# Performance work log

Measured on AMD Instinct MI355X. Metric: run time of the kernel, lower is better.

## Reference

```python
import jax, jax.numpy as jnp
import numpy as np

HEADS = 16
EMBED = 1024
HEAD_DIM = EMBED // HEADS


def setup_inputs() -> dict:
    key = jax.random.key(0)
    ks = jax.random.split(key, 10)
    B, SQ, SKV = 2, 2048, 2048
    s = 1.0 / np.sqrt(HEAD_DIM)
    sd = 1.0 / np.sqrt(EMBED)
    return {
        "queries": jax.random.normal(ks[0], (B, SQ, EMBED), jnp.float32),
        "values": jax.random.normal(ks[1], (B, SKV, EMBED), jnp.float32),
        "heads": HEADS,
        "Wv": jax.random.normal(ks[2], (HEAD_DIM, HEAD_DIM), jnp.float32) * s,
        "bv": jax.random.normal(ks[3], (HEAD_DIM,), jnp.float32) * 0.02,
        "Wk": jax.random.normal(ks[4], (HEAD_DIM, HEAD_DIM), jnp.float32) * s,
        "bk": jax.random.normal(ks[5], (HEAD_DIM,), jnp.float32) * 0.02,
        "Wq": jax.random.normal(ks[6], (HEAD_DIM, HEAD_DIM), jnp.float32) * s,
        "bq": jax.random.normal(ks[7], (HEAD_DIM,), jnp.float32) * 0.02,
        "Wd": jax.random.normal(ks[8], (EMBED, EMBED), jnp.float32) * sd,
        "bd": jax.random.normal(ks[9], (EMBED,), jnp.float32) * 0.02,
    }


def reference(queries, values, heads, Wv, bv, Wk, bk, Wq, bq, Wd, bd):
    n, sq, e = queries.shape
    skv = values.shape[1]
    d = e // heads
    # reshape to per-head layout [b, s, h, d]
    q_in = queries.reshape(n, sq, heads, d)
    v_in = values.reshape(n, skv, heads, d)
    # shared per-head linear projections (torch Linear: x @ W.T + b)
    v = jnp.einsum("bshd,ed->bshe", v_in, Wv) + bv
    # quirk preserved: keys computed from the ALREADY-PROJECTED values
    k = jnp.einsum("bshd,ed->bshe", v, Wk) + bk
    q = jnp.einsum("bshd,ed->bshe", q_in, Wq) + bq
    # full O(n^2) score matrix [b, h, sq, skv] (as in source)
    scores = jnp.einsum("bqhd,bkhd->bhqk", q, k) / jnp.sqrt(jnp.asarray(d, q.dtype))
    attn = jax.nn.softmax(scores, axis=-1)
    out = jnp.einsum("bhqk,bkhd->bqhd", attn, v).reshape(n, sq, e)
    return out @ Wd.T + bd
```

## Files before the change

kernel.cpp:

```cpp
#include <hip/hip_runtime.h>
#include <hip/hip_bf16.h>
#include <hip/hip_fp16.h>
#include <math.h>

typedef _Float16 f16;
typedef _Float16 f16x8 __attribute__((ext_vector_type(8)));
typedef _Float16 f16x4 __attribute__((ext_vector_type(4)));
typedef _Float16 f16x2 __attribute__((ext_vector_type(2)));
typedef unsigned short u16x8v __attribute__((ext_vector_type(8)));
typedef float f32x4 __attribute__((ext_vector_type(4)));

namespace {
constexpr int B = 2;
constexpr int H = 16;
constexpr int S = 2048;
constexpr int D = 64;
constexpr int E = 1024;
constexpr float QSCALE = 0.125f * 1.4426950408889634f;
}

#define GLOBAL_LOAD_LDS16(gp, lp)                                              \
  __builtin_amdgcn_global_load_lds(                                            \
      (const __attribute__((address_space(1))) void*)(gp),                     \
      (__attribute__((address_space(3))) void*)(lp), 16, 0, 0)

__global__ __launch_bounds__(256) void prep(const float* __restrict__ Wd, f16* __restrict__ wd16,
                                            const float* __restrict__ Wk, const float* __restrict__ Wv,
                                            const float* __restrict__ bv, const float* __restrict__ bk,
                                            float* __restrict__ Wkv, float* __restrict__ bkv) {
  if (blockIdx.x < 1024) {
    const int i = blockIdx.x * 256 + threadIdx.x;
    const float4 f = ((const float4*)Wd)[i];
    f16x4 o;
    o.x = (f16)f.x; o.y = (f16)f.y; o.z = (f16)f.z; o.w = (f16)f.w;
    *(f16x4*)(wd16 + 4 * (size_t)i) = o;
  } else {
    const int g = (blockIdx.x - 1024) * 256 + threadIdx.x;
    const int i = g >> 6, j = g & 63;
    float s = 0.f;
#pragma unroll 16
    for (int d = 0; d < 64; ++d) s = fmaf(Wk[i * 64 + d], Wv[d * 64 + j], s);
    Wkv[g] = s;
    if (g < 64) {
      float bb = bk[g];
#pragma unroll 16
      for (int d = 0; d < 64; ++d) bb = fmaf(Wk[g * 64 + d], bv[d], bb);
      bkv[g] = bb;
    }
  }
}

__global__ __launch_bounds__(256) void proj3_mfma(const float* __restrict__ xq,
                                                  const float* __restrict__ xv,
                                                  const float* __restrict__ Wq,
                                                  const float* __restrict__ bq,
                                                  const float* __restrict__ Wv,
                                                  const float* __restrict__ bv,
                                                  const float* __restrict__ Wkv,
                                                  const float* __restrict__ bkv,
                                                  f16* __restrict__ qp,
                                                  f16* __restrict__ vtp,
                                                  f16* __restrict__ kp) {
  __shared__ f16 tb[16 * 16 * 68];
  const int which = blockIdx.y;
  const float* x = which ? xv : xq;

  const int t = threadIdx.x, lane = t & 63, w = t >> 6;
  const int l15 = lane & 15, quad = lane >> 4;
  const int m0 = (blockIdx.x * 4 + w) * 64;

  f16x8 af[4][2];
#pragma unroll
  for (int mt = 0; mt < 4; ++mt)
#pragma unroll
    for (int kc = 0; kc < 2; ++kc) {
      const float* g = x + (size_t)(m0 + mt * 16 + l15) * 64 + kc * 32 + quad * 8;
      const float4 a = *(const float4*)g, b2 = *(const float4*)(g + 4);
      f16x8 v;
      v[0]=(f16)a.x; v[1]=(f16)a.y; v[2]=(f16)a.z; v[3]=(f16)a.w;
      v[4]=(f16)b2.x; v[5]=(f16)b2.y; v[6]=(f16)b2.z; v[7]=(f16)b2.w;
      af[mt][kc] = v;
    }

  const int npass = which ? 2 : 1;
  for (int pass = 0; pass < npass; ++pass) {
    const float* W    = which ? (pass ? Wkv : Wv) : Wq;
    const float* bias = which ? (pass ? bkv : bv) : bq;
    const bool vpass  = (which == 1) && (pass == 0);
    const bool kpass  = (which == 1) && (pass == 1);
    const float scale = which ? 1.0f : QSCALE;

    f16x8 wf[4][2];
#pragma unroll
    for (int nt = 0; nt < 4; ++nt)
#pragma unroll
      for (int kc = 0; kc < 2; ++kc) {
        const float* g = W + (size_t)(nt * 16 + l15) * 64 + kc * 32 + quad * 8;
        const float4 a = *(const float4*)g, b2 = *(const float4*)(g + 4);
        f16x8 v;
        v[0]=(f16)a.x; v[1]=(f16)a.y; v[2]=(f16)a.z; v[3]=(f16)a.w;
        v[4]=(f16)b2.x; v[5]=(f16)b2.y; v[6]=(f16)b2.z; v[7]=(f16)b2.w;
        wf[nt][kc] = v;
      }

    f32x4 acc[4][4];
#pragma unroll
    for (int nt = 0; nt < 4; ++nt)
#pragma unroll
      for (int mt = 0; mt < 4; ++mt) acc[nt][mt] = (f32x4){0.f, 0.f, 0.f, 0.f};
#pragma unroll
    for (int kc = 0; kc < 2; ++kc)
#pragma unroll
      for (int nt = 0; nt < 4; ++nt)
#pragma unroll
        for (int mt = 0; mt < 4; ++mt)
          acc[nt][mt] = __builtin_amdgcn_mfma_f32_16x16x32_f16(wf[nt][kc], af[mt][kc], acc[nt][mt], 0, 0, 0);

    float4 bl4[4];
#pragma unroll
    for (int nt = 0; nt < 4; ++nt) bl4[nt] = *(const float4*)&bias[nt * 16 + quad * 4];

#pragma unroll
    for (int mt = 0; mt < 4; ++mt) {
      const int g = m0 + mt * 16 + l15;
#pragma unroll
      for (int nt = 0; nt < 4; ++nt) {
        const float p0 = (acc[nt][mt][0] + bl4[nt].x) * scale;
        const float p1 = (acc[nt][mt][1] + bl4[nt].y) * scale;
        const float p2 = (acc[nt][mt][2] + bl4[nt].z) * scale;
        const float p3 = (acc[nt][mt][3] + bl4[nt].w) * scale;
        union { f16x4 v4; f16x2 hh[2]; } u;
        u.hh[0] = __builtin_bit_cast(f16x2, __builtin_amdgcn_cvt_pkrtz(p0, p1));
        u.hh[1] = __builtin_bit_cast(f16x2, __builtin_amdgcn_cvt_pkrtz(p2, p3));
        if (vpass) {
#pragma unroll
          for (int r = 0; r < 4; ++r)
            tb[(l15 * 64 + nt * 16 + quad * 4 + r) * 16 + w * 4 + mt] = u.v4[r];
        } else if (kpass) {
          *(f16x4*)&tb[(l15 * 16 + w * 4 + mt) * 68 + nt * 16 + quad * 4] = u.v4;
        } else {
          *(f16x4*)(qp + (size_t)g * 64 + nt * 16 + quad * 4) = u.v4;
        }
      }
    }

    if (vpass) {
      __syncthreads();
      const int bsb = blockIdx.x * 16;
      const int bb = bsb >> 11;
      const int sb = bsb & 2047;
      const int off = sb & 63;
      const int poff = (off & 32) | ((off & 16) >> 2);
      const int col0 = (sb - off) + poff;
#pragma unroll
      for (int k2 = 0; k2 < 4; ++k2) {
        const int pi = t * 4 + k2;
        const int h = pi >> 6, d = pi & 63;
        const f16x8 lo = *(const f16x8*)&tb[pi * 16];
        const f16x8 hi = *(const f16x8*)&tb[pi * 16 + 8];
        f16* orow = vtp + ((size_t)(bb * H + h) * 64 + d) * S + col0;
        f16x4 g0, g1, g2, g3;
#pragma unroll
        for (int j = 0; j < 4; ++j) { g0[j]=lo[j]; g1[j]=lo[4+j]; g2[j]=hi[j]; g3[j]=hi[4+j]; }
        *(f16x4*)(orow + 0)  = g0;
        *(f16x4*)(orow + 8)  = g1;
        *(f16x4*)(orow + 16) = g2;
        *(f16x4*)(orow + 24) = g3;
      }
      __syncthreads();
    } else if (kpass) {
      __syncthreads();
      const int bsb = blockIdx.x * 16;
      const int bb = bsb >> 11;
      const int sblk = bsb & 2047;
      const int h = t >> 4, sl = t & 15;
      f16* dst = kp + ((size_t)(bb * H + h) * S + sblk + sl) * 64;
      const f16* src = &tb[t * 68];
#pragma unroll
      for (int c = 0; c < 8; ++c)
        *(f16x8*)(dst + c * 8) = *(const f16x8*)(src + c * 8);
    }
  }
}

__global__ __launch_bounds__(512, 4) void attn_mfma(const f16* __restrict__ qp,
                                                    const f16* __restrict__ kp,
                                                    const f16* __restrict__ vtp,
                                                    f16* __restrict__ ao) {
  __shared__ f16 smem[4][64 * 64];
  const int t = threadIdx.x, lane = t & 63, w = t >> 6;
  const int l15 = lane & 15, quad = lane >> 4;
  const int wq = w >> 1, wk = w & 1;
  const int bh = blockIdx.x;
  const int b = bh >> 4, h = bh & 15;
  const int q0 = blockIdx.y * 128;
  const f16* kbase = kp + (size_t)bh * S * D;
  const f16* vtbase = vtp + (size_t)bh * 64 * S;

  const int row1 = t >> 3;
  const size_t koff = (size_t)row1 * D + (((t & 7) ^ (row1 & 7)) * 8);
  const size_t voff = (size_t)row1 * S + (((t & 7) ^ (row1 & 7)) * 8);

  f16x8 qf[2][2];
#pragma unroll
  for (int mt = 0; mt < 2; ++mt)
#pragma unroll
    for (int kc = 0; kc < 2; ++kc)
      qf[mt][kc] = *(const f16x8*)(qp +
          ((size_t)(b * S + q0 + wq * 32 + mt * 16 + l15) * H + h) * 64 + kc * 32 + quad * 8);

  f16x8 vb4;
#pragma unroll
  for (int j = 0; j < 8; ++j) vb4[j] = (l15 == 0) ? (f16)1.0f : (f16)0.0f;

  f32x4 O[2][5];
#pragma unroll
  for (int mt = 0; mt < 2; ++mt)
#pragma unroll
    for (int nt = 0; nt < 5; ++nt) O[mt][nt] = (f32x4){0.f, 0.f, 0.f, 0.f};

#define ISSUE_TILE(tt, buf)                                                    \
  {                                                                            \
    const f16* gk = kbase + (size_t)(tt) * (64 * D);                           \
    GLOBAL_LOAD_LDS16(gk + koff, &smem[buf][t * 8]);                           \
    const f16* gv = vtbase + (size_t)(tt) * 64;                                \
    GLOBAL_LOAD_LDS16(gv + voff, &smem[2 + (buf)][t * 8]);                     \
  }

  ISSUE_TILE(0, 0);

  for (int kt = 0; kt < S / 64; ++kt) {
    const int rb = kt & 1;
    __asm__ volatile("s_waitcnt vmcnt(0)" ::: "memory");
    __builtin_amdgcn_s_barrier();
    __asm__ volatile("" ::: "memory");
    if (kt + 1 < S / 64) ISSUE_TILE(kt + 1, rb ^ 1);

    f32x4 sc[2][2];
#pragma unroll
    for (int ntl = 0; ntl < 2; ++ntl)
#pragma unroll
      for (int mt = 0; mt < 2; ++mt) sc[ntl][mt] = (f32x4){0.f, 0.f, 0.f, 0.f};
    __builtin_amdgcn_s_setprio(1);
#pragma unroll
    for (int kcq = 0; kcq < 2; ++kcq)
#pragma unroll
      for (int ntl = 0; ntl < 2; ++ntl) {
        const f16x8 kf = *(const f16x8*)&smem[rb][(wk * 32 + ntl * 16 + l15) * 64 + (((kcq * 4 + quad) ^ (l15 & 7)) * 8)];
#pragma unroll
        for (int mt = 0; mt < 2; ++mt)
          sc[ntl][mt] = __builtin_amdgcn_mfma_f32_16x16x32_f16(kf, qf[mt][kcq], sc[ntl][mt], 0, 0, 0);
      }
    __builtin_amdgcn_s_setprio(0);

    f16x8 pa[2];
#pragma unroll
    for (int mt = 0; mt < 2; ++mt) {
      const f32x4 s0 = sc[0][mt], s1 = sc[1][mt];
      union { f16x8 v8; f16x2 hh[4]; } u;
      u.hh[0] = __builtin_bit_cast(f16x2, __builtin_amdgcn_cvt_pkrtz(
          __builtin_amdgcn_exp2f(s0[0]), __builtin_amdgcn_exp2f(s0[1])));
      u.hh[1] = __builtin_bit_cast(f16x2, __builtin_amdgcn_cvt_pkrtz(
          __builtin_amdgcn_exp2f(s0[2]), __builtin_amdgcn_exp2f(s0[3])));
      u.hh[2] = __builtin_bit_cast(f16x2, __builtin_amdgcn_cvt_pkrtz(
          __builtin_amdgcn_exp2f(s1[0]), __builtin_amdgcn_exp2f(s1[1])));
      u.hh[3] = __builtin_bit_cast(f16x2, __builtin_amdgcn_cvt_pkrtz(
          __builtin_amdgcn_exp2f(s1[2]), __builtin_amdgcn_exp2f(s1[3])));
      pa[mt] = u.v8;
    }

    __builtin_amdgcn_s_setprio(1);
#pragma unroll
    for (int nt = 0; nt < 4; ++nt) {
      const f16x8 vbf = *(const f16x8*)&smem[2 + rb][(nt * 16 + l15) * 64 + (((wk * 4 + quad) ^ (l15 & 7)) * 8)];
#pragma unroll
      for (int mt = 0; mt < 2; ++mt)
        O[mt][nt] = __builtin_amdgcn_mfma_f32_16x16x32_f16(pa[mt], vbf, O[mt][nt], 0, 0, 0);
    }
#pragma unroll
    for (int mt = 0; mt < 2; ++mt)
      O[mt][4] = __builtin_amdgcn_mfma_f32_16x16x32_f16(pa[mt], vb4, O[mt][4], 0, 0, 0);
    __builtin_amdgcn_s_setprio(0);
  }
#undef ISSUE_TILE

  float* red = (float*)&smem[0][0];
  __syncthreads();
  if (wk) {
    float* dst = red + (size_t)(wq * 64 + lane) * 20;
#pragma unroll
    for (int nt = 0; nt < 5; ++nt)
#pragma unroll
      for (int r = 0; r < 4; ++r) dst[nt * 4 + r] = O[0][nt][r];
  }
  __syncthreads();
  if (!wk) {
    const float* src = red + (size_t)(wq * 64 + lane) * 20;
#pragma unroll
    for (int nt = 0; nt < 5; ++nt)
#pragma unroll
      for (int r = 0; r < 4; ++r) O[0][nt][r] += src[nt * 4 + r];
  }
  __syncthreads();
  if (wk) {
    float* dst = red + (size_t)(wq * 64 + lane) * 20;
#pragma unroll
    for (int nt = 0; nt < 5; ++nt)
#pragma unroll
      for (int r = 0; r < 4; ++r) dst[nt * 4 + r] = O[1][nt][r];
  }
  __syncthreads();
  if (!wk) {
    const float* src = red + (size_t)(wq * 64 + lane) * 20;
#pragma unroll
    for (int nt = 0; nt < 5; ++nt)
#pragma unroll
      for (int r = 0; r < 4; ++r) O[1][nt][r] += src[nt * 4 + r];

#pragma unroll
    for (int mt = 0; mt < 2; ++mt)
#pragma unroll
      for (int r = 0; r < 4; ++r) {
        const float l = __shfl(O[mt][4][r], quad << 4, 64);
        const float inv = 1.f / l;
        const int row = q0 + wq * 32 + mt * 16 + quad * 4 + r;
        f16* o = ao + ((size_t)b * S + row) * E + h * D;
#pragma unroll
        for (int nt = 0; nt < 4; ++nt)
          o[nt * 16 + l15] = (f16)(O[mt][nt][r] * inv);
      }
  }
}

__global__ __launch_bounds__(256) void dense_mfma(const f16* __restrict__ A,
                                                  const f16* __restrict__ Wd16,
                                                  const float* __restrict__ bd,
                                                  float* __restrict__ out) {
  __shared__ f16 as[3][128 * 64];
  __shared__ f16 bs[3][64 * 64];
  const int t = threadIdx.x;
  const int lane = t & 63;
  const int w = t >> 6;
  const int l15 = lane & 15;
  const int quad = lane >> 4;
  const int m0 = blockIdx.x * 128;
  const int n0 = blockIdx.y * 64;
  const int wm = (w >> 1) * 64, wn = (w & 1) * 32;

  const int srow = (lane >> 3);
  const int schunk = (lane & 7) ^ srow;
  const f16* ga0 = A    + (size_t)(m0 + w * 32 + srow) * E + schunk * 8;
  const f16* gb0 = Wd16 + (size_t)(n0 + w * 16 + srow) * E + schunk * 8;

  constexpr int NT = E / 64;

#define ISSUE_D(tt, ib)                                                        \
  {                                                                            \
    _Pragma("unroll")                                                          \
    for (int i = 0; i < 4; ++i)                                                \
      GLOBAL_LOAD_LDS16(ga0 + (size_t)(i * 8) * E + (tt) * 64,                 \
                        &as[ib][(w * 32 + i * 8) * 64]);                       \
    _Pragma("unroll")                                                          \
    for (int i = 0; i < 2; ++i)                                                \
      GLOBAL_LOAD_LDS16(gb0 + (size_t)(i * 8) * E + (tt) * 64,                 \
                        &bs[ib][(w * 16 + i * 8) * 64]);                       \
  }

  f32x4 acc[4][2];
#pragma unroll
  for (int mt = 0; mt < 4; ++mt)
#pragma unroll
    for (int nt = 0; nt < 2; ++nt) acc[mt][nt] = (f32x4){0.f, 0.f, 0.f, 0.f};

  ISSUE_D(0, 0);
  ISSUE_D(1, 1);
  __asm__ volatile("s_waitcnt vmcnt(6)" ::: "memory");
  __builtin_amdgcn_s_barrier();
  __asm__ volatile("" ::: "memory");

  int rb = 0, ib = 2;
  for (int kt = 0; kt < NT; ++kt) {
    {
      const int tt = (kt + 2 < NT) ? (kt + 2) : (NT - 1);
      ISSUE_D(tt, ib);
    }
    f16x8 af[4][2];
#pragma unroll
    for (int mt = 0; mt < 4; ++mt)
#pragma unroll
      for (int kc = 0; kc < 2; ++kc)
        af[mt][kc] = *(const f16x8*)&as[rb][(wm + mt * 16 + l15) * 64 + (((kc * 4 + quad) ^ (l15 & 7)) * 8)];
#pragma unroll
    for (int kc = 0; kc < 2; ++kc)
#pragma unroll
      for (int nt = 0; nt < 2; ++nt) {
        const f16x8 bf = *(const f16x8*)&bs[rb][(wn + nt * 16 + l15) * 64 + (((kc * 4 + quad) ^ (l15 & 7)) * 8)];
#pragma unroll
        for (int mt = 0; mt < 4; ++mt)
          acc[mt][nt] = __builtin_amdgcn_mfma_f32_16x16x32_f16(af[mt][kc], bf, acc[mt][nt], 0, 0, 0);
      }
    __asm__ volatile("s_waitcnt vmcnt(6)" ::: "memory");
    __builtin_amdgcn_s_barrier();
    __asm__ volatile("" ::: "memory");
    rb = (rb + 1 >= 3) ? 0 : rb + 1;
    ib = (ib + 1 >= 3) ? 0 : ib + 1;
  }
#undef ISSUE_D

#pragma unroll
  for (int nt = 0; nt < 2; ++nt) {
    const int col = n0 + wn + nt * 16 + l15;
    const float bdv = bd[col];
#pragma unroll
    for (int mt = 0; mt < 4; ++mt)
#pragma unroll
      for (int r = 0; r < 4; ++r)
        out[(size_t)(m0 + wm + mt * 16 + quad * 4 + r) * E + col] = acc[mt][nt][r] + bdv;
  }
}

extern "C" void kernel_launch(void* const* d_in, const int* in_sizes, int n_in,
                              void* d_out, int out_size, void* d_ws, size_t ws_size,
                              hipStream_t stream) {
  const float* queries = (const float*)d_in[0];
  const float* values  = (const float*)d_in[1];
  const float* Wv = (const float*)d_in[3];
  const float* bv = (const float*)d_in[4];
  const float* Wk = (const float*)d_in[5];
  const float* bk = (const float*)d_in[6];
  const float* Wq = (const float*)d_in[7];
  const float* bq = (const float*)d_in[8];
  const float* Wd = (const float*)d_in[9];
  const float* bd = (const float*)d_in[10];
  float* out = (float*)d_out;

  char* ws = (char*)d_ws;
  f16* qp    = (f16*)(ws);
  f16* kp    = (f16*)(ws + 8u * 1024 * 1024);
  f16* vtp   = (f16*)(ws + 16u * 1024 * 1024);
  f16* ao    = (f16*)(ws + 24u * 1024 * 1024);
  f16* wd16  = (f16*)(ws + 32u * 1024 * 1024);
  float* wkv = (float*)(ws + 34u * 1024 * 1024);
  float* bkv = (float*)(ws + 34u * 1024 * 1024 + 16384);
  (void)ws_size; (void)in_sizes; (void)n_in; (void)out_size;

  prep<<<1040, 256, 0, stream>>>(Wd, wd16, Wk, Wv, bv, bk, wkv, bkv);
  proj3_mfma<<<dim3(256, 2), 256, 0, stream>>>(queries, values, Wq, bq, Wv, bv, wkv, bkv, qp, vtp, kp);
  attn_mfma<<<dim3(B * H, S / 128), 512, 0, stream>>>(qp, kp, vtp, ao);
  dense_mfma<<<dim3(B * S / 128, E / 64), 256, 0, stream>>>(ao, wd16, bd, out);
}
```

Measured before the change: 175.5 us.

## Triple-buffer K/V tiles and prefetch next K fragments into registers

```diff
diff --git a/kernel.cpp b/kernel.cpp
--- a/kernel.cpp
+++ b/kernel.cpp
@@ -187,7 +187,7 @@
                                                     const f16* __restrict__ kp,
                                                     const f16* __restrict__ vtp,
                                                     f16* __restrict__ ao) {
-  __shared__ f16 smem[4][64 * 64];
+  __shared__ f16 smem[6][64 * 64];
   const int t = threadIdx.x, lane = t & 63, w = t >> 6;
   const int l15 = lane & 15, quad = lane >> 4;
   const int wq = w >> 1, wk = w & 1;
@@ -219,22 +219,41 @@
 #pragma unroll
     for (int nt = 0; nt < 5; ++nt) O[mt][nt] = (f32x4){0.f, 0.f, 0.f, 0.f};
 
+  int kofs[2][2];
+#pragma unroll
+  for (int kcq = 0; kcq < 2; ++kcq)
+#pragma unroll
+    for (int ntl = 0; ntl < 2; ++ntl)
+      kofs[kcq][ntl] = (wk * 32 + ntl * 16 + l15) * 64 + (((kcq * 4 + quad) ^ (l15 & 7)) * 8);
+
 #define ISSUE_TILE(tt, buf)                                                    \
   {                                                                            \
     const f16* gk = kbase + (size_t)(tt) * (64 * D);                           \
     GLOBAL_LOAD_LDS16(gk + koff, &smem[buf][t * 8]);                           \
     const f16* gv = vtbase + (size_t)(tt) * 64;                                \
-    GLOBAL_LOAD_LDS16(gv + voff, &smem[2 + (buf)][t * 8]);                     \
-  }
+    GLOBAL_LOAD_LDS16(gv + voff, &smem[3 + (buf)][t * 8]);                     \
+  }
+
+  f16x8 kfA[2][2], kfB[2][2];
+  constexpr int NT = S / 64;
 
   ISSUE_TILE(0, 0);
-
-  for (int kt = 0; kt < S / 64; ++kt) {
-    const int rb = kt & 1;
-    __asm__ volatile("s_waitcnt vmcnt(0)" ::: "memory");
-    __builtin_amdgcn_s_barrier();
-    __asm__ volatile("" ::: "memory");
-    if (kt + 1 < S / 64) ISSUE_TILE(kt + 1, rb ^ 1);
+  ISSUE_TILE(1, 1);
+  __asm__ volatile("s_waitcnt vmcnt(2)" ::: "memory");
+  __builtin_amdgcn_s_barrier();
+  __asm__ volatile("" ::: "memory");
+#pragma unroll
+  for (int kcq = 0; kcq < 2; ++kcq)
+#pragma unroll
+    for (int ntl = 0; ntl < 2; ++ntl)
+      kfA[kcq][ntl] = *(const f16x8*)&smem[0][kofs[kcq][ntl]];
+
+  auto STEP = [&](int kt, f16x8 (&kfc)[2][2], f16x8 (&kfn)[2][2]) {
+    {
+      const int tt = (kt + 2 < NT) ? (kt + 2) : (NT - 1);
+      const int ib = (kt + 2) % 3;
+      ISSUE_TILE(tt, ib);
+    }
 
     f32x4 sc[2][2];
 #pragma unroll
@@ -245,12 +264,10 @@
 #pragma unroll
     for (int kcq = 0; kcq < 2; ++kcq)
 #pragma unroll
-      for (int ntl = 0; ntl < 2; ++ntl) {
-        const f16x8 kf = *(const f16x8*)&smem[rb][(wk * 32 + ntl * 16 + l15) * 64 + (((kcq * 4 + quad) ^ (l15 & 7)) * 8)];
+      for (int ntl = 0; ntl < 2; ++ntl)
 #pragma unroll
         for (int mt = 0; mt < 2; ++mt)
-          sc[ntl][mt] = __builtin_amdgcn_mfma_f32_16x16x32_f16(kf, qf[mt][kcq], sc[ntl][mt], 0, 0, 0);
-      }
+          sc[ntl][mt] = __builtin_amdgcn_mfma_f32_16x16x32_f16(kfc[kcq][ntl], qf[mt][kcq], sc[ntl][mt], 0, 0, 0);
     __builtin_amdgcn_s_setprio(0);
 
     f16x8 pa[2];
@@ -269,10 +286,23 @@
       pa[mt] = u.v8;
     }
 
+    __asm__ volatile("s_waitcnt vmcnt(2)" ::: "memory");
+    __builtin_amdgcn_s_barrier();
+    __asm__ volatile("" ::: "memory");
+    {
+      const f16* kb1 = &smem[(kt + 1) % 3][0];
+#pragma unroll
+      for (int kcq = 0; kcq < 2; ++kcq)
+#pragma unroll
+        for (int ntl = 0; ntl < 2; ++ntl)
+          kfn[kcq][ntl] = *(const f16x8*)(kb1 + kofs[kcq][ntl]);
+    }
+
     __builtin_amdgcn_s_setprio(1);
+    const f16* vbuf = &smem[3 + (kt % 3)][0];
 #pragma unroll
     for (int nt = 0; nt < 4; ++nt) {
-      const f16x8 vbf = *(const f16x8*)&smem[2 + rb][(nt * 16 + l15) * 64 + (((wk * 4 + quad) ^ (l15 & 7)) * 8)];
+      const f16x8 vbf = *(const f16x8*)(vbuf + (nt * 16 + l15) * 64 + (((wk * 4 + quad) ^ (l15 & 7)) * 8));
 #pragma unroll
       for (int mt = 0; mt < 2; ++mt)
         O[mt][nt] = __builtin_amdgcn_mfma_f32_16x16x32_f16(pa[mt], vbf, O[mt][nt], 0, 0, 0);
@@ -281,6 +311,14 @@
     for (int mt = 0; mt < 2; ++mt)
       O[mt][4] = __builtin_amdgcn_mfma_f32_16x16x32_f16(pa[mt], vb4, O[mt][4], 0, 0, 0);
     __builtin_amdgcn_s_setprio(0);
+
+    __builtin_amdgcn_s_barrier();
+    __asm__ volatile("" ::: "memory");
+  };
+
+  for (int kt2 = 0; kt2 < NT; kt2 += 2) {
+    STEP(kt2 + 0, kfA, kfB);
+    STEP(kt2 + 1, kfB, kfA);
   }
 #undef ISSUE_TILE
 
```

Result: no change. 174.3 us (-0.7%).
